# Kernel optimization log

Measured on AMD Instinct MI355X. Metric: run time of the kernel, lower is better.

## Reference

```python
import jax, jax.numpy as jnp
import numpy as np


def setup_inputs() -> dict:
    key = jax.random.key(0)
    ks = jax.random.split(key, 5)
    N, T, D, H = 256, 64, 1024, 1024
    x = jax.random.normal(ks[0], (N, T, D), dtype=jnp.float32)
    A = jax.random.normal(ks[1], (N, H, 4, 4), dtype=jnp.float32)
    Wx = jax.random.normal(ks[2], (D, 4 * H), dtype=jnp.float32) / np.sqrt(D)
    Wh = jax.random.normal(ks[3], (H, 4 * H), dtype=jnp.float32) / np.sqrt(H)
    Wattn = jax.random.normal(ks[4], (H, 4 * H), dtype=jnp.float32) / np.sqrt(H)
    b = jnp.zeros((4 * H,), dtype=jnp.float32)
    return {"x": x, "A": A, "Wx": Wx, "Wh": Wh, "Wattn": Wattn, "b": b}


def reference(x, A, Wx, Wh, Wattn, b):
    # x: (N,T,D); A: (N,H,4,4); Wx: (D,4H); Wh,Wattn: (H,4H); b: (4H,)
    N, T, D = x.shape
    H = A.shape[1]
    A_flat = A.reshape(N, H, 16)                 # 16 = 4*4 spatial keys
    h0 = A_flat.mean(axis=2)                     # (N,H); c0 = h0
    scale = 1.0 / jnp.sqrt(jnp.asarray(H, dtype=x.dtype))

    def step(carry, xt):
        prev_h, prev_c = carry
        # scaled dot-product attention over 16 spatial positions
        scores = jnp.einsum('nh,nhk->nk', prev_h, A_flat) * scale   # (N,16)
        w = jax.nn.softmax(scores, axis=1)                           # (N,16)
        attn = jnp.einsum('nhk,nk->nh', A_flat, w)                   # (N,H)
        # LSTM gates with attention term
        a = xt @ Wx + prev_h @ Wh + attn @ Wattn + b                 # (N,4H)
        ai, af, ao, ag = jnp.split(a, 4, axis=1)
        i = jax.nn.sigmoid(ai)
        f = jax.nn.sigmoid(af)
        o = jax.nn.sigmoid(ao)
        g = jnp.tanh(ag)
        next_c = f * prev_c + i * g
        next_h = o * jnp.tanh(next_c)
        return (next_h, next_c), next_h

    xs = jnp.swapaxes(x, 0, 1)                   # (T,N,D)
    _, hs = jax.lax.scan(step, (h0, h0), xs)     # hs: (T,N,H)
    return jnp.swapaxes(hs, 0, 1)                # (N,T,H)
```

## Files before the change

### kernel.cpp

```cpp
#include <hip/hip_runtime.h>
#include <math.h>

#define NB 256
#define TT 64
#define DD 1024
#define HH 1024
#define FOURH 4096
#define KTOT 3072
#define KT16 192
#define P1 (NB * FOURH)

#define AF_LVL 786432ull
#define BF_LVL 12582912ull
#define SPLIT_SCALE 2048.0f
#define INV_SPLIT (1.0f / 2048.0f)

typedef _Float16 f16x8 __attribute__((ext_vector_type(8)));
typedef float f32x4 __attribute__((ext_vector_type(4)));
typedef float f32x16 __attribute__((ext_vector_type(16)));

__device__ __forceinline__ unsigned short f2h(float f) {
    _Float16 h = (_Float16)f;
    unsigned short u;
    __builtin_memcpy(&u, &h, 2);
    return u;
}
__device__ __forceinline__ float h2f(unsigned short u) {
    _Float16 h;
    __builtin_memcpy(&h, &u, 2);
    return (float)h;
}
__device__ __forceinline__ void split2(float f, unsigned short& hi, unsigned short& lo) {
    hi = f2h(f);
    lo = f2h((f - h2f(hi)) * SPLIT_SCALE);
}

__device__ __forceinline__ size_t aoff(int lvl, int mt, int kt, int lane) {
    return ((size_t)((lvl * 8 + mt) * KT16 + kt) * 64 + lane) * 8;
}
__device__ __forceinline__ size_t boff(int lvl, int ct, int kt, int lane) {
    return ((size_t)((lvl * 128 + ct) * KT16 + kt) * 64 + lane) * 8;
}

__device__ __forceinline__ void write_frag8(unsigned short* __restrict__ Af, int n, int k8, const float* v) {
    int mt = n >> 5, kt = k8 >> 4;
    int lane = (n & 31) + 32 * ((k8 >> 3) & 1);
    unsigned short s[8][2];
#pragma unroll
    for (int i = 0; i < 8; ++i) split2(v[i], s[i][0], s[i][1]);
#pragma unroll
    for (int lvl = 0; lvl < 2; ++lvl) {
        uint4 p;
        p.x = (unsigned)s[0][lvl] | ((unsigned)s[1][lvl] << 16);
        p.y = (unsigned)s[2][lvl] | ((unsigned)s[3][lvl] << 16);
        p.z = (unsigned)s[4][lvl] | ((unsigned)s[5][lvl] << 16);
        p.w = (unsigned)s[6][lvl] | ((unsigned)s[7][lvl] << 16);
        *reinterpret_cast<uint4*>(Af + aoff(lvl, mt, kt, lane)) = p;
    }
}

__global__ __launch_bounds__(256) void wsplit_kernel(const float* __restrict__ Wx,
                                                     const float* __restrict__ Wh,
                                                     const float* __restrict__ Wattn,
                                                     unsigned short* __restrict__ Bf) {
    __shared__ float tile[32][33];
    int k0 = blockIdx.x * 32, j0 = blockIdx.y * 32;
    int t = threadIdx.x;
    int rl = t >> 3, c4 = (t & 7) * 4;
    int seg = k0 >> 10;
    const float* W = (seg == 0) ? Wx : (seg == 1) ? Wh : Wattn;
    const float4 v = *reinterpret_cast<const float4*>(W + (size_t)((k0 & 1023) + rl) * FOURH + j0 + c4);
    tile[rl][c4 + 0] = v.x; tile[rl][c4 + 1] = v.y; tile[rl][c4 + 2] = v.z; tile[rl][c4 + 3] = v.w;
    __syncthreads();
    int jl = t >> 3, k4 = (t & 7) * 4;
    unsigned short s[4][2];
#pragma unroll
    for (int i = 0; i < 4; ++i) split2(tile[k4 + i][jl], s[i][0], s[i][1]);
    int j = j0 + jl;
    int kg = k0 + k4;
    int ct = j >> 5, kt = kg >> 4;
    int lane = (j & 31) + 32 * ((kg >> 3) & 1);
    int sub = kg & 7;
#pragma unroll
    for (int lvl = 0; lvl < 2; ++lvl) {
        uint2 p;
        p.x = (unsigned)s[0][lvl] | ((unsigned)s[1][lvl] << 16);
        p.y = (unsigned)s[2][lvl] | ((unsigned)s[3][lvl] << 16);
        *reinterpret_cast<uint2*>(Bf + boff(lvl, ct, kt, lane) + sub) = p;
    }
}

__device__ __forceinline__ void attn_phase(const float* __restrict__ A, int n, int tid,
                                           const float* hsh, float* ash, float* red2) {
    int lane = tid & 63, wave = tid >> 6;
    const float* An = A + (size_t)n * HH * 16;
    float areg[2][16];
    float part[16];
#pragma unroll
    for (int k = 0; k < 16; ++k) part[k] = 0.f;
#pragma unroll
    for (int i = 0; i < 2; ++i) {
        int hh = tid + i * 512;
        float hv = hsh[hh];
        const float* ap = An + (size_t)hh * 16;
#pragma unroll
        for (int k = 0; k < 16; ++k) {
            float av = ap[k];
            areg[i][k] = av;
            part[k] += hv * av;
        }
    }
#pragma unroll
    for (int k = 0; k < 16; ++k) {
        float v = part[k];
#pragma unroll
        for (int off = 32; off > 0; off >>= 1) v += __shfl_down(v, off);
        if (lane == 0) red2[wave * 16 + k] = v;
    }
    __syncthreads();
    float w[16];
    float mx = -1e30f;
#pragma unroll
    for (int k = 0; k < 16; ++k) {
        float s = 0.f;
#pragma unroll
        for (int q = 0; q < 8; ++q) s += red2[q * 16 + k];
        s *= 0.03125f;
        w[k] = s;
        mx = fmaxf(mx, s);
    }
    float sum = 0.f;
#pragma unroll
    for (int k = 0; k < 16; ++k) {
        w[k] = expf(w[k] - mx);
        sum += w[k];
    }
    float inv = 1.0f / sum;
#pragma unroll
    for (int k = 0; k < 16; ++k) w[k] *= inv;
#pragma unroll
    for (int i = 0; i < 2; ++i) {
        float s = 0.f;
#pragma unroll
        for (int k = 0; k < 16; ++k) s += areg[i][k] * w[k];
        ash[tid + i * 512] = s;
    }
}

__device__ __forceinline__ void write_state_frags(unsigned short* __restrict__ Af,
                                                  const float* __restrict__ x,
                                                  const float* hsh, const float* ash,
                                                  int n, int tnext, int tid) {
    if (tid >= 128) return;
    int k8 = tid * 8;
    float v[8];
#pragma unroll
    for (int i = 0; i < 8; ++i) v[i] = hsh[k8 + i];
    write_frag8(Af, n, 1024 + k8, v);
#pragma unroll
    for (int i = 0; i < 8; ++i) v[i] = ash[k8 + i];
    write_frag8(Af, n, 2048 + k8, v);
    if (tnext < TT) {
        const float4* xp = reinterpret_cast<const float4*>(x + ((size_t)n * TT + tnext) * DD + k8);
        float4 x0 = xp[0], x1 = xp[1];
        v[0] = x0.x; v[1] = x0.y; v[2] = x0.z; v[3] = x0.w;
        v[4] = x1.x; v[5] = x1.y; v[6] = x1.z; v[7] = x1.w;
        write_frag8(Af, n, k8, v);
    }
}

__global__ __launch_bounds__(512) void initk(const float* __restrict__ A,
                                             const float* __restrict__ x,
                                             float* __restrict__ c,
                                             unsigned short* __restrict__ Af) {
    int n = blockIdx.x, tid = threadIdx.x;
    __shared__ float hsh[HH], ash[HH];
    __shared__ float red2[128];
#pragma unroll
    for (int i = 0; i < 2; ++i) {
        int hh = tid + i * 512;
        const float* ap = A + ((size_t)n * HH + hh) * 16;
        float s = 0.f;
#pragma unroll
        for (int k = 0; k < 16; ++k) s += ap[k];
        s *= (1.0f / 16.0f);
        c[(size_t)n * HH + hh] = s;
        hsh[hh] = s;
    }
    __syncthreads();
    attn_phase(A, n, tid, hsh, ash, red2);
    __syncthreads();
    write_state_frags(Af, x, hsh, ash, n, 0, tid);
}

#define DEPTH 4
#define KTPB 48

#define LOADB(slot, kt)                                                                        \
    {                                                                                          \
        _Pragma("unroll") for (int lvl = 0; lvl < 2; ++lvl) {                                  \
            _Pragma("unroll") for (int mi = 0; mi < 2; ++mi)                                   \
                FA[slot][lvl][mi] = *reinterpret_cast<const uint4*>(pa[lvl][mi] + (size_t)(kt) * 512); \
            FB[slot][lvl] = *reinterpret_cast<const uint4*>(pb[lvl] + (size_t)(kt) * 512);     \
        }                                                                                      \
    }

__global__ __launch_bounds__(512, 2) void gemm_mfma(const unsigned short* __restrict__ Af,
                                                    const unsigned short* __restrict__ Bf,
                                                    float* __restrict__ apart) {
    int tid = threadIdx.x;
    int l = tid & 63, w = tid >> 6;
    int wm = w & 3, wn = w >> 2;
    int bid = blockIdx.x;
    int id = (bid & 7) * 32 + (bid >> 3);
    int colb = id & 63, z = id >> 6;
    int kt0 = z * KTPB;

    const unsigned short* pa[2][2];
    const unsigned short* pb[2];
#pragma unroll
    for (int lvl = 0; lvl < 2; ++lvl) {
#pragma unroll
        for (int mi = 0; mi < 2; ++mi)
            pa[lvl][mi] = Af + aoff(lvl, wm * 2 + mi, kt0, l);
        pb[lvl] = Bf + boff(lvl, colb * 2 + wn, kt0, l);
    }

    f32x16 accH[2] = {};
    f32x16 accM[2] = {};
    uint4 FA[DEPTH][2][2];
    uint4 FB[DEPTH][2];

    LOADB(0, 0)
    LOADB(1, 1)
    LOADB(2, 2)

#pragma unroll 4
    for (int kt = 0; kt < KTPB; ++kt) {
        int pf = (kt + 3 < KTPB) ? kt + 3 : KTPB - 1;
        LOADB((kt + 3) & 3, pf)
        int s = kt & 3;
        f16x8 b0 = __builtin_bit_cast(f16x8, FB[s][0]);
        f16x8 b1 = __builtin_bit_cast(f16x8, FB[s][1]);
#pragma unroll
        for (int mi = 0; mi < 2; ++mi) {
            f16x8 a0 = __builtin_bit_cast(f16x8, FA[s][0][mi]);
            f16x8 a1 = __builtin_bit_cast(f16x8, FA[s][1][mi]);
            accH[mi] = __builtin_amdgcn_mfma_f32_32x32x16_f16(a0, b0, accH[mi], 0, 0, 0);
            accM[mi] = __builtin_amdgcn_mfma_f32_32x32x16_f16(a0, b1, accM[mi], 0, 0, 0);
            accM[mi] = __builtin_amdgcn_mfma_f32_32x32x16_f16(a1, b0, accM[mi], 0, 0, 0);
        }
    }

    float* plane = apart + (size_t)z * P1;
    int col = colb * 64 + wn * 32 + (l & 31);
#pragma unroll
    for (int mi = 0; mi < 2; ++mi) {
        int rbase = (wm * 2 + mi) * 32 + (l >> 5) * 4;
#pragma unroll
        for (int r = 0; r < 16; ++r) {
            int row = rbase + (r & 3) + 8 * (r >> 2);
            plane[(size_t)row * FOURH + col] = accH[mi][r] + accM[mi][r] * INV_SPLIT;
        }
    }
}

__global__ __launch_bounds__(512) void pointwise(const float* __restrict__ apart,
                                                 const float* __restrict__ bias,
                                                 const float* __restrict__ A,
                                                 const float* __restrict__ x,
                                                 float* __restrict__ c,
                                                 float* __restrict__ out,
                                                 unsigned short* __restrict__ Af, int t) {
    int n = blockIdx.x, tid = threadIdx.x;
    __shared__ float hsh[HH], ash[HH];
    __shared__ float red2[128];
    const float* ap = apart + (size_t)n * FOURH;
#pragma unroll
    for (int i = 0; i < 2; ++i) {
        int hh = i * 512 + tid;
        float g4[4];
#pragma unroll
        for (int g = 0; g < 4; ++g) {
            int j = g * 1024 + hh;
            g4[g] = bias[j] + ap[j] + ap[(size_t)P1 + j] + ap[2 * (size_t)P1 + j] + ap[3 * (size_t)P1 + j];
        }
        float ig = 1.f / (1.f + expf(-g4[0]));
        float fg = 1.f / (1.f + expf(-g4[1]));
        float og = 1.f / (1.f + expf(-g4[2]));
        float gg = tanhf(g4[3]);
        float cn = fg * c[(size_t)n * HH + hh] + ig * gg;
        float hn = og * tanhf(cn);
        c[(size_t)n * HH + hh] = cn;
        out[((size_t)n * TT + t) * HH + hh] = hn;
        hsh[hh] = hn;
    }
    __syncthreads();
    attn_phase(A, n, tid, hsh, ash, red2);
    __syncthreads();
    write_state_frags(Af, x, hsh, ash, n, t + 1, tid);
}

extern "C" void kernel_launch(void* const* d_in, const int* in_sizes, int n_in,
                              void* d_out, int out_size, void* d_ws, size_t ws_size,
                              hipStream_t stream) {
    const float* x     = (const float*)d_in[0];
    const float* A     = (const float*)d_in[1];
    const float* Wx    = (const float*)d_in[2];
    const float* Wh    = (const float*)d_in[3];
    const float* Wattn = (const float*)d_in[4];
    const float* b     = (const float*)d_in[5];
    float* out = (float*)d_out;

    unsigned short* Bf = (unsigned short*)d_ws;
    unsigned short* Af = Bf + 2 * BF_LVL;
    float* apart = (float*)(Af + 2 * AF_LVL);
    float* c = apart + 4 * (size_t)P1;

    wsplit_kernel<<<dim3(KTOT / 32, FOURH / 32), 256, 0, stream>>>(Wx, Wh, Wattn, Bf);
    initk<<<NB, 512, 0, stream>>>(A, x, c, Af);

    for (int t = 0; t < TT; ++t) {
        gemm_mfma<<<256, 512, 0, stream>>>(Af, Bf, apart);
        pointwise<<<NB, 512, 0, stream>>>(apart, b, A, x, c, out, Af, t);
    }
}
```

Before: 2.826 ms.

## Stage weight fragments through LDS with async global_load_lds and vectorize pointwise

The GEMM kernel no longer has each wave load its B (weight) fragments from global memory into a register prefetch ring. The workgroup now cooperatively stages B chunks into double-buffered shared memory via global_load_lds and reads them from LDS, while A fragments are loaded directly each k-step. This aims to cut duplicate global traffic for B across the row waves, at the cost of barriers per chunk, 64KB LDS and dropping the 2-blocks-per-CU occupancy hint. The pointwise kernel is vectorized to float2 and the fragment writes are spread across more threads.

New measurement: 3.365 ms. +19.1%, slower.

```diff
diff --git a/kernel.cpp b/kernel.cpp
--- a/kernel.cpp
+++ b/kernel.cpp
@@ -151,16 +151,18 @@
                                                   const float* __restrict__ x,
                                                   const float* hsh, const float* ash,
                                                   int n, int tnext, int tid) {
-    if (tid >= 128) return;
-    int k8 = tid * 8;
+    int seg = tid >> 7;
+    int k8 = (tid & 127) * 8;
     float v[8];
-#pragma unroll
-    for (int i = 0; i < 8; ++i) v[i] = hsh[k8 + i];
-    write_frag8(Af, n, 1024 + k8, v);
-#pragma unroll
-    for (int i = 0; i < 8; ++i) v[i] = ash[k8 + i];
-    write_frag8(Af, n, 2048 + k8, v);
-    if (tnext < TT) {
+    if (seg == 0) {
+#pragma unroll
+        for (int i = 0; i < 8; ++i) v[i] = hsh[k8 + i];
+        write_frag8(Af, n, 1024 + k8, v);
+    } else if (seg == 1) {
+#pragma unroll
+        for (int i = 0; i < 8; ++i) v[i] = ash[k8 + i];
+        write_frag8(Af, n, 2048 + k8, v);
+    } else if (seg == 2 && tnext < TT) {
         const float4* xp = reinterpret_cast<const float4*>(x + ((size_t)n * TT + tnext) * DD + k8);
         float4 x0 = xp[0], x1 = xp[1];
         v[0] = x0.x; v[1] = x0.y; v[2] = x0.z; v[3] = x0.w;
@@ -193,21 +195,26 @@
     write_state_frags(Af, x, hsh, ash, n, 0, tid);
 }
 
-#define DEPTH 4
 #define KTPB 48
-
-#define LOADB(slot, kt)                                                                        \
-    {                                                                                          \
-        _Pragma("unroll") for (int lvl = 0; lvl < 2; ++lvl) {                                  \
-            _Pragma("unroll") for (int mi = 0; mi < 2; ++mi)                                   \
-                FA[slot][lvl][mi] = *reinterpret_cast<const uint4*>(pa[lvl][mi] + (size_t)(kt) * 512); \
-            FB[slot][lvl] = *reinterpret_cast<const uint4*>(pb[lvl] + (size_t)(kt) * 512);     \
+#define CH 8
+#define NCHUNK (KTPB / CH)
+
+#define STAGE(bufidx, c)                                                                       \
+    if ((c) < NCHUNK) {                                                                        \
+        int ktg = kt0 + (c) * CH + w;                                                          \
+        _Pragma("unroll") for (int j = 0; j < 4; ++j) {                                        \
+            const unsigned short* gp = Bf + boff(j & 1, colb * 2 + (j >> 1), ktg, l);          \
+            __builtin_amdgcn_global_load_lds(                                                  \
+                (const __attribute__((address_space(1))) unsigned int*)gp,                     \
+                (__attribute__((address_space(3))) unsigned int*)&Bsm[(bufidx)][(w * 4 + j) * 512], \
+                16, 0, 0);                                                                     \
         }                                                                                      \
     }
 
-__global__ __launch_bounds__(512, 2) void gemm_mfma(const unsigned short* __restrict__ Af,
-                                                    const unsigned short* __restrict__ Bf,
-                                                    float* __restrict__ apart) {
+__global__ __launch_bounds__(512) void gemm_mfma(const unsigned short* __restrict__ Af,
+                                                 const unsigned short* __restrict__ Bf,
+                                                 float* __restrict__ apart) {
+    __shared__ __align__(16) short Bsm[2][32 * 512];
     int tid = threadIdx.x;
     int l = tid & 63, w = tid >> 6;
     int wm = w & 3, wn = w >> 2;
@@ -217,39 +224,43 @@
     int kt0 = z * KTPB;
 
     const unsigned short* pa[2][2];
-    const unsigned short* pb[2];
-#pragma unroll
-    for (int lvl = 0; lvl < 2; ++lvl) {
+#pragma unroll
+    for (int lvl = 0; lvl < 2; ++lvl)
 #pragma unroll
         for (int mi = 0; mi < 2; ++mi)
             pa[lvl][mi] = Af + aoff(lvl, wm * 2 + mi, kt0, l);
-        pb[lvl] = Bf + boff(lvl, colb * 2 + wn, kt0, l);
-    }
 
     f32x16 accH[2] = {};
     f32x16 accM[2] = {};
-    uint4 FA[DEPTH][2][2];
-    uint4 FB[DEPTH][2];
-
-    LOADB(0, 0)
-    LOADB(1, 1)
-    LOADB(2, 2)
-
-#pragma unroll 4
-    for (int kt = 0; kt < KTPB; ++kt) {
-        int pf = (kt + 3 < KTPB) ? kt + 3 : KTPB - 1;
-        LOADB((kt + 3) & 3, pf)
-        int s = kt & 3;
-        f16x8 b0 = __builtin_bit_cast(f16x8, FB[s][0]);
-        f16x8 b1 = __builtin_bit_cast(f16x8, FB[s][1]);
-#pragma unroll
-        for (int mi = 0; mi < 2; ++mi) {
-            f16x8 a0 = __builtin_bit_cast(f16x8, FA[s][0][mi]);
-            f16x8 a1 = __builtin_bit_cast(f16x8, FA[s][1][mi]);
-            accH[mi] = __builtin_amdgcn_mfma_f32_32x32x16_f16(a0, b0, accH[mi], 0, 0, 0);
-            accM[mi] = __builtin_amdgcn_mfma_f32_32x32x16_f16(a0, b1, accM[mi], 0, 0, 0);
-            accM[mi] = __builtin_amdgcn_mfma_f32_32x32x16_f16(a1, b0, accM[mi], 0, 0, 0);
+
+    STAGE(0, 0)
+    __syncthreads();
+
+    for (int c = 0; c < NCHUNK; ++c) {
+        int cur = c & 1;
+        STAGE(cur ^ 1, c + 1)
+#pragma unroll
+        for (int ktc = 0; ktc < CH; ++ktc) {
+            int kt = c * CH + ktc;
+            uint4 a00 = *reinterpret_cast<const uint4*>(pa[0][0] + (size_t)kt * 512);
+            uint4 a01 = *reinterpret_cast<const uint4*>(pa[0][1] + (size_t)kt * 512);
+            uint4 a10 = *reinterpret_cast<const uint4*>(pa[1][0] + (size_t)kt * 512);
+            uint4 a11 = *reinterpret_cast<const uint4*>(pa[1][1] + (size_t)kt * 512);
+            const short* bp = &Bsm[cur][(ktc * 4 + wn * 2) * 512 + l * 8];
+            f16x8 b0 = *reinterpret_cast<const f16x8*>(bp);
+            f16x8 b1 = *reinterpret_cast<const f16x8*>(bp + 512);
+            f16x8 a0m0 = __builtin_bit_cast(f16x8, a00);
+            f16x8 a0m1 = __builtin_bit_cast(f16x8, a01);
+            f16x8 a1m0 = __builtin_bit_cast(f16x8, a10);
+            f16x8 a1m1 = __builtin_bit_cast(f16x8, a11);
+            accH[0] = __builtin_amdgcn_mfma_f32_32x32x16_f16(a0m0, b0, accH[0], 0, 0, 0);
+            accM[0] = __builtin_amdgcn_mfma_f32_32x32x16_f16(a0m0, b1, accM[0], 0, 0, 0);
+            accM[0] = __builtin_amdgcn_mfma_f32_32x32x16_f16(a1m0, b0, accM[0], 0, 0, 0);
+            accH[1] = __builtin_amdgcn_mfma_f32_32x32x16_f16(a0m1, b0, accH[1], 0, 0, 0);
+            accM[1] = __builtin_amdgcn_mfma_f32_32x32x16_f16(a0m1, b1, accM[1], 0, 0, 0);
+            accM[1] = __builtin_amdgcn_mfma_f32_32x32x16_f16(a1m1, b0, accM[1], 0, 0, 0);
         }
+        __syncthreads();
     }
 
     float* plane = apart + (size_t)z * P1;
@@ -276,25 +287,42 @@
     __shared__ float hsh[HH], ash[HH];
     __shared__ float red2[128];
     const float* ap = apart + (size_t)n * FOURH;
-#pragma unroll
-    for (int i = 0; i < 2; ++i) {
-        int hh = i * 512 + tid;
-        float g4[4];
-#pragma unroll
-        for (int g = 0; g < 4; ++g) {
-            int j = g * 1024 + hh;
-            g4[g] = bias[j] + ap[j] + ap[(size_t)P1 + j] + ap[2 * (size_t)P1 + j] + ap[3 * (size_t)P1 + j];
+    int hh2 = tid * 2;
+    float2 g2[4];
+#pragma unroll
+    for (int g = 0; g < 4; ++g) {
+        int j = g * 1024 + hh2;
+        float2 s = *reinterpret_cast<const float2*>(bias + j);
+#pragma unroll
+        for (int zz = 0; zz < 4; ++zz) {
+            float2 p = *reinterpret_cast<const float2*>(ap + (size_t)zz * P1 + j);
+            s.x += p.x; s.y += p.y;
         }
-        float ig = 1.f / (1.f + expf(-g4[0]));
-        float fg = 1.f / (1.f + expf(-g4[1]));
-        float og = 1.f / (1.f + expf(-g4[2]));
-        float gg = tanhf(g4[3]);
-        float cn = fg * c[(size_t)n * HH + hh] + ig * gg;
-        float hn = og * tanhf(cn);
-        c[(size_t)n * HH + hh] = cn;
-        out[((size_t)n * TT + t) * HH + hh] = hn;
-        hsh[hh] = hn;
-    }
+        g2[g] = s;
+    }
+    float2 cold = *reinterpret_cast<const float2*>(c + (size_t)n * HH + hh2);
+    float2 hn2;
+    {
+        float ig = 1.f / (1.f + expf(-g2[0].x));
+        float fg = 1.f / (1.f + expf(-g2[1].x));
+        float og = 1.f / (1.f + expf(-g2[2].x));
+        float gg = tanhf(g2[3].x);
+        float cn = fg * cold.x + ig * gg;
+        hn2.x = og * tanhf(cn);
+        cold.x = cn;
+    }
+    {
+        float ig = 1.f / (1.f + expf(-g2[0].y));
+        float fg = 1.f / (1.f + expf(-g2[1].y));
+        float og = 1.f / (1.f + expf(-g2[2].y));
+        float gg = tanhf(g2[3].y);
+        float cn = fg * cold.y + ig * gg;
+        hn2.y = og * tanhf(cn);
+        cold.y = cn;
+    }
+    *reinterpret_cast<float2*>(c + (size_t)n * HH + hh2) = cold;
+    *reinterpret_cast<float2*>(out + ((size_t)n * TT + t) * HH + hh2) = hn2;
+    *reinterpret_cast<float2*>(&hsh[hh2]) = hn2;
     __syncthreads();
     attn_phase(A, n, tid, hsh, ash, red2);
     __syncthreads();
```
